# Optimization experiments

Measured on AMD Instinct MI355X. Metric: run time of the kernel, lower is better.

## Reference

```python
import jax, jax.numpy as jnp
import numpy as np

GRID = (128, 128, 128)
CENTER = np.array([0.0, 0.0, 0.0], dtype=np.float32)
SIZE = np.array([214.0, 214.0, 214.0], dtype=np.float32)
N_LORS = 65536
_CRYSTAL = SIZE[2] / GRID[2]
KERNEL_WIDTH = float(np.sqrt(_CRYSTAL * _CRYSTAL / np.pi))  # TOR gaussian sigma


def _make_lors(key, n, s):
    # rows: x1, y1, z1, x2, y2, z2 ; main direction along the 3rd coordinate
    k1, k2 = jax.random.split(key)
    trans = jax.random.uniform(k1, (4, n), jnp.float32, -0.45 * s, 0.45 * s)
    jit = jax.random.uniform(k2, (2, n), jnp.float32, -0.02 * s, 0.02 * s)
    half = 0.5 * s
    return jnp.stack([trans[0], trans[1], -half + jit[0],
                      trans[2], trans[3], half + jit[1]]).astype(jnp.float32)


def _project_bp(lors, image, grid, center, size, sigma):
    """TOR (tube-of-response) projection + listmode backprojection.
    lors: [N,6]; image shape == grid; main ray axis = last grid axis.
    Returns (line_integrals [N], backprojection volume grid)."""
    n0, n1, n2 = grid
    center = jnp.asarray(center, jnp.float32)
    size = jnp.asarray(size, jnp.float32)
    vox = size / jnp.array(grid, jnp.float32)
    xmin = center[0] - 0.5 * size[0]
    ymin = center[1] - 0.5 * size[1]
    zmin = center[2] - 0.5 * size[2]
    p1, p2 = lors[:, 0:3], lors[:, 3:6]
    d = p2 - p1
    L = jnp.sqrt(jnp.sum(d * d, axis=1))                    # [N]
    dz = d[:, 2]
    dz = jnp.where(jnp.abs(dz) < 1e-6, 1e-6, dz)
    zc = zmin + (jnp.arange(n2, dtype=jnp.float32) + 0.5) * vox[2]  # [K]
    t = (zc[None, :] - p1[:, 2:3]) / dz[:, None]            # [N,K] ray param per slice
    xs = p1[:, 0:1] + t * d[:, 0:1]                         # [N,K]
    ys = p1[:, 1:2] + t * d[:, 1:2]
    fi = (xs - xmin) / vox[0] - 0.5
    fj = (ys - ymin) / vox[1] - 0.5
    i0 = jnp.round(fi).astype(jnp.int32)
    j0 = jnp.round(fj).astype(jnp.int32)
    off = jnp.arange(-1, 2, dtype=jnp.int32)                # 3x3 in-plane TOR window
    oi = jnp.repeat(off, 3)                                  # [9]
    oj = jnp.tile(off, 3)                                    # [9]
    ii = i0[..., None] + oi                                  # [N,K,9]
    jj = j0[..., None] + oj
    inb = ((ii >= 0) & (ii < n0) & (jj >= 0) & (jj < n1)
           & (t[..., None] >= 0.0) & (t[..., None] <= 1.0))
    iic = jnp.clip(ii, 0, n0 - 1)
    jjc = jnp.clip(jj, 0, n1 - 1)
    dxv = (xmin + (iic.astype(jnp.float32) + 0.5) * vox[0]) - xs[..., None]
    dyv = (ymin + (jjc.astype(jnp.float32) + 0.5) * vox[1]) - ys[..., None]
    w = jnp.exp(-(dxv * dxv + dyv * dyv) / (2.0 * sigma * sigma))
    w = jnp.where(inb, w, 0.0)                               # [N,K,9]
    dl = vox[2] * L / jnp.abs(dz)                            # path length per slice [N]
    kk = jnp.broadcast_to(jnp.arange(n2, dtype=jnp.int32)[None, :, None], ii.shape)
    vals = image[iic, jjc, kk]                               # gather [N,K,9]
    proj = jnp.sum(w * vals, axis=(1, 2)) * dl               # [N]
    # listmode MLEM backprojection of 1/projection along same TOR weights
    contrib = w * (dl / (proj + 1e-8))[:, None, None]        # [N,K,9]
    flat = (iic * n1 + jjc) * n2 + kk
    bp = jnp.zeros(n0 * n1 * n2, jnp.float32).at[flat.reshape(-1)].add(
        contrib.reshape(-1)).reshape(n0, n1, n2)
    return proj, bp


def setup_inputs() -> dict:
    key = jax.random.key(0)
    kimg, keff, kx, ky, kz = jax.random.split(key, 5)
    image = jax.random.uniform(kimg, GRID, jnp.float32, 0.5, 1.5)
    effmap = jax.random.uniform(keff, GRID, jnp.float32, 0.5, 1.5)
    s = float(SIZE[0])
    return {
        'image': image,
        'efficiency_map': effmap,
        'xlors': _make_lors(kx, N_LORS, s),
        'ylors': _make_lors(ky, N_LORS, s),
        'zlors': _make_lors(kz, N_LORS, s),
    }


def reference(image, efficiency_map, xlors, ylors, zlors):
    g0, g1, g2 = GRID
    sigma = KERNEL_WIDTH
    imgz = image
    imgx = jnp.transpose(imgz, (2, 0, 1))
    imgy = jnp.transpose(imgz, (1, 0, 2))
    # stored as [6, N] -> [N, 6]
    xl, yl, zl = xlors.T, ylors.T, zlors.T
    pz, bpz = _project_bp(zl, imgz, GRID, CENTER, SIZE, sigma)
    gridx = (g0, g2, g1)
    px, bpx = _project_bp(xl, imgx, gridx, CENTER[[0, 2, 1]], SIZE[[0, 2, 1]], sigma)
    bpxt = jnp.transpose(bpx, (1, 2, 0))
    gridy = (g1, g2, g0)
    py, bpy = _project_bp(yl, imgy, gridy, CENTER[[1, 2, 0]], SIZE[[1, 2, 0]], sigma)
    bpyt = jnp.transpose(bpy, (1, 0, 2))
    return imgz / (efficiency_map + 1e-8) * (bpxt + bpyt + bpz)
```

## Files before the change

kernel.cpp:

```cpp
#include <hip/hip_runtime.h>
#include <hip/hip_fp16.h>
#include <math.h>

#define NLOR  65536
#define NG    128
#define PLANE (NG * NG)
#define NSUB  2
#define KG    8
#define NKG   (NG / KG)

#define VOX    1.671875f
#define XMIN  (-107.0f)
#define C2     1.57079632679f
#define C2L    2.26618007f

#define FPSCALE    8388608.0f
#define INVFPSCALE (1.0f / 8388608.0f)

#define PLP    129

#define PRM_STRIDE 8

typedef _Float16 h2v __attribute__((ext_vector_type(2)));

#if defined(__has_builtin)
#if __has_builtin(__builtin_amdgcn_fdot2)
#define HAVE_FDOT2 1
#endif
#endif

__device__ __forceinline__ float fdot2w(unsigned w, h2v wt, float c)
{
#ifdef HAVE_FDOT2
    return __builtin_amdgcn_fdot2(__builtin_bit_cast(h2v, w), wt, c, false);
#else
    const __half2 h = *reinterpret_cast<const __half2*>(&w);
    const float2 f = __half22float2(h);
    return c + (float)wt.x * f.x + (float)wt.y * f.y;
#endif
}

template<int SP, int SQ, int SR, int CONTIG>
__device__ __forceinline__ void permute_half_body(
    const float* __restrict__ in, __half* __restrict__ out,
    int b, float (*tile)[33])
{
    const int c0 = blockIdx.x * 32;
    const int r0 = blockIdx.y * 32;
    const int tx = threadIdx.x, ty = threadIdx.y;

#pragma unroll
    for (int m = 0; m < 4; ++m) {
        const int C = c0 + tx;
        const int R = r0 + ty + 8 * m;
        const int P = (CONTIG == 0) ? C : b;
        const int Q = (CONTIG == 0) ? b : C;
        tile[ty + 8 * m][tx] = in[P * SP + Q * SQ + R * SR];
    }
    __syncthreads();
#pragma unroll
    for (int m = 0; m < 4; ++m) {
        const int R = r0 + tx;
        const int C = c0 + ty + 8 * m;
        const int P = (CONTIG == 0) ? C : b;
        const int Q = (CONTIG == 0) ? b : C;
        const int o = P * PLANE + Q * NG + R;
        out[o] = __float2half(tile[tx][ty + 8 * m]);
    }
}

__global__ __launch_bounds__(256)
void perm_img2(const float* __restrict__ image,
               __half* __restrict__ imgPz, __half* __restrict__ imgPx,
               const float* __restrict__ zl, const float* __restrict__ yl,
               const float* __restrict__ xl,
               float* __restrict__ prmz, float* __restrict__ prmy,
               float* __restrict__ prmx)
{
    __shared__ float tile[32][33];
    const int b = blockIdx.z;
    if (b < 128) {
        permute_half_body<1, 16384, 128, 0>(image, imgPz, b, tile);
        return;
    }
    if (b < 256) {
        permute_half_body<128, 1, 16384, 1>(image, imgPx, b - 128, tile);
        return;
    }
    const int linear = (b - 256) * 16 + blockIdx.y * 4 + blockIdx.x;
    const int gid = linear * 256 + threadIdx.y * 32 + threadIdx.x;
    const int f   = gid >> 16;
    const int lor = gid & (NLOR - 1);
    const float* lors = (f == 0) ? zl : (f == 1) ? yl : xl;
    float* prm        = (f == 0) ? prmz : (f == 1) ? prmy : prmx;

    const float p1x = lors[0 * NLOR + lor];
    const float p1y = lors[1 * NLOR + lor];
    const float p1z = lors[2 * NLOR + lor];
    const float dx  = lors[3 * NLOR + lor] - p1x;
    const float dy  = lors[4 * NLOR + lor] - p1y;
    float dz = lors[5 * NLOR + lor] - p1z;
    dz = (fabsf(dz) < 1e-6f) ? 1e-6f : dz;
    const float rdz = 1.0f / dz;

    const float t0 = (XMIN + 0.5f * VOX - p1z) * rdz;
    const float dt = VOX * rdz;
    float u0 = (fmaf(t0, dx, p1x) - XMIN) * (1.0f / VOX) - 0.5f;
    float v0 = (fmaf(t0, dy, p1y) - XMIN) * (1.0f / VOX) - 0.5f;
    float du = dx * rdz;
    float dv = dy * rdz;
    if (f == 1) {
        float tmp = u0; u0 = v0; v0 = tmp;
        tmp = du; du = dv; dv = tmp;
    }
    float4* p4 = (float4*)(prm + (size_t)lor * PRM_STRIDE);
    p4[0] = make_float4(u0, du, v0, dv);
    p4[1] = make_float4(t0, dt, 0.0f, 0.0f);
}

template<int NS>
__device__ __forceinline__ void proj_body(
    const float* const* prmv, const unsigned int* __restrict__ imgP,
    float* const* p8v, unsigned int* plE, unsigned int* plO)
{
    const int g     = blockIdx.x;
    const int chunk = blockIdx.y;
    const int tid   = threadIdx.x;
    const int lor0  = chunk * 2048 + tid;
    const float k0  = (float)(g * KG);

    float tA[2 * NS], uA[2 * NS], vA[2 * NS], dtA[2 * NS], duA[2 * NS], dvA[2 * NS], sA[2 * NS];
#pragma unroll
    for (int s = 0; s < 2 * NS; ++s) {
        const float* prm = prmv[s >> 1];
        const int lor = lor0 + (s & 1) * 1024;
        const float4* p4 = (const float4*)(prm + (size_t)lor * PRM_STRIDE);
        const float4 a = p4[0];
        const float4 b = p4[1];
        tA[s] = fmaf(k0, b.y, b.x);  dtA[s] = b.y;
        uA[s] = fmaf(k0, a.y, a.x);  duA[s] = a.y;
        vA[s] = fmaf(k0, a.w, a.z);  dvA[s] = a.w;
        sA[s] = 0.0f;
    }

    for (int st = 0; st < KG; ++st) {
        const int k = g * KG + st;
        const unsigned* srcw = imgP + k * (NG * 64);
        const uint4* src = (const uint4*)srcw;
        uint4* dstE = (uint4*)plE;
        uint4* dstO = (uint4*)plO;
        for (int i = tid; i < (NG * 64) / 4; i += 1024) {
            const uint4 a = src[i];
            const unsigned nxt = srcw[4 * i + 4];
            uint4 o;
            o.x = (a.x >> 16) | (a.y << 16);
            o.y = (a.y >> 16) | (a.z << 16);
            o.z = (a.z >> 16) | (a.w << 16);
            o.w = (a.w >> 16) | (nxt << 16);
            dstE[i] = a;
            dstO[i] = o;
        }
        __syncthreads();

        const float fst = (float)st;
#pragma unroll
        for (int s = 0; s < 2 * NS; ++s) {
            const float t = fmaf(fst, dtA[s], tA[s]);
            const float u = fmaf(fst, duA[s], uA[s]);
            const float v = fmaf(fst, dvA[s], vA[s]);
            const float fi = rintf(u);
            const float fj = rintf(v);
            const int i0 = (int)fi;
            const int j0 = (int)fj;
            const float mi = fi - u;
            const float mj = fj - v;
            const float ci = -C2L * mi,  cj = -C2L * mj;
            const float a0i = ci * mi,   a0j = cj * mj;
            const float gi = ci + ci,    gj = cj + cj;
            const float ki = a0i - C2L,  kj = a0j - C2L;
            const float exm = __builtin_amdgcn_exp2f(ki - gi);
            const float ex0 = __builtin_amdgcn_exp2f(a0i);
            const float exq = __builtin_amdgcn_exp2f(ki + gi);
            const float eym = __builtin_amdgcn_exp2f(kj - gj);
            const float ey0 = __builtin_amdgcn_exp2f(a0j);
            const float eyq = __builtin_amdgcn_exp2f(kj + gj);

            h2v wLo; wLo.x = (_Float16)eym; wLo.y = (_Float16)ey0;
            h2v wHi; wHi.x = (_Float16)eyq; wHi.y = (_Float16)0.0f;

            const int w  = min(max((j0 - 1) >> 1, 0), 62);
            const int ib = min(max(i0 - 1, 0), 125);
            const unsigned* pp = (j0 & 1) ? plE : plO;

            const float exv[3] = {exm, ex0, exq};
            float acc = 0.0f;
#pragma unroll
            for (int a = 0; a < 3; ++a) {
                const int rowb = (ib + a) << 6;
                const unsigned Aw = pp[rowb + w];
                const unsigned Bw = pp[rowb + w + 1];
                float rd = fdot2w(Bw, wHi, 0.0f);
                rd = fdot2w(Aw, wLo, rd);
                acc = fmaf(exv[a], rd, acc);
            }
            const bool tin = (t >= 0.0f) && (t <= 1.0f);
            sA[s] += tin ? acc : 0.0f;
        }
        __syncthreads();
    }
#pragma unroll
    for (int s = 0; s < NS; ++s) {
        p8v[s][g * NLOR + lor0]        = sA[2 * s];
        p8v[s][g * NLOR + lor0 + 1024] = sA[2 * s + 1];
    }
}

__global__ __launch_bounds__(1024, 8)
void proj_all(const float* __restrict__ prmz, const float* __restrict__ prmy,
              const float* __restrict__ prmx,
              const unsigned int* __restrict__ imgPz, const unsigned int* __restrict__ imgPx,
              float* __restrict__ p8z, float* __restrict__ p8y,
              float* __restrict__ p8x)
{
    __shared__ unsigned int plE[NG * 64];
    __shared__ unsigned int plO[NG * 64];
    if (blockIdx.z == 0) {
        const float* prmv[2] = {prmz, prmy};
        float* p8v[2] = {p8z, p8y};
        proj_body<2>(prmv, imgPz, p8v, plE, plO);
    } else {
        const float* prmv[1] = {prmx};
        float* p8v[1] = {p8x};
        proj_body<1>(prmv, imgPx, p8v, plE, plO);
    }
}

__global__ __launch_bounds__(256)
void reduce_cf3(const float* __restrict__ zl, const float* __restrict__ yl,
                const float* __restrict__ xl,
                const float* __restrict__ p8z, const float* __restrict__ p8y,
                const float* __restrict__ p8x,
                float* __restrict__ prmz, float* __restrict__ prmy,
                float* __restrict__ prmx)
{
    const int which = blockIdx.y;
    const float* lors  = (which == 0) ? zl  : (which == 1) ? yl  : xl;
    const float* part8 = (which == 0) ? p8z : (which == 1) ? p8y : p8x;
    float*       prm   = (which == 0) ? prmz : (which == 1) ? prmy : prmx;

    const int lor = blockIdx.x * 256 + threadIdx.x;
    float s = 0.0f;
#pragma unroll
    for (int g = 0; g < NKG; ++g) s += part8[g * NLOR + lor];

    const float p1x = lors[0 * NLOR + lor];
    const float p1y = lors[1 * NLOR + lor];
    const float p1z = lors[2 * NLOR + lor];
    const float dx  = lors[3 * NLOR + lor] - p1x;
    const float dy  = lors[4 * NLOR + lor] - p1y;
    const float dz0 = lors[5 * NLOR + lor] - p1z;
    const float L = sqrtf(dx * dx + dy * dy + dz0 * dz0);
    const float adz = fmaxf(fabsf(dz0), 1e-6f);
    const float dl = VOX * L / adz;
    prm[(size_t)lor * PRM_STRIDE + 6] = (dl / (s * dl + 1e-8f)) * FPSCALE;
}

__device__ __forceinline__ void bp_deposit(const float* __restrict__ prm,
    int lor, float fk, unsigned int* __restrict__ pl)
{
    const float4* p4 = (const float4*)(prm + (size_t)lor * PRM_STRIDE);
    const float4 a = p4[0];
    const float4 b = p4[1];
    const float t = fmaf(fk, b.y, b.x);
    const float u = fmaf(fk, a.y, a.x);
    const float v = fmaf(fk, a.w, a.z);
    const float fi = rintf(u);
    const float fj = rintf(v);
    const float cfs = ((t >= 0.0f) && (t <= 1.0f)) ? b.z : 0.0f;

    const float mi = fi - u;
    const float mj = fj - v;
    const float ci = -C2L * mi,  cj = -C2L * mj;
    const float a0i = ci * mi,   a0j = cj * mj;
    const float gi = ci + ci,    gj = cj + cj;
    const float ki = a0i - C2L,  kj = a0j - C2L;

    const float ex0 = __builtin_amdgcn_exp2f(a0i) * cfs;
    const float exm = __builtin_amdgcn_exp2f(ki - gi) * cfs;
    const float exq = __builtin_amdgcn_exp2f(ki + gi) * cfs;
    const float ey0 = __builtin_amdgcn_exp2f(a0j);
    const float eym = __builtin_amdgcn_exp2f(kj - gj);
    const float eyq = __builtin_amdgcn_exp2f(kj + gj);

    const float fib = __builtin_amdgcn_fmed3f(fi, 1.0f, 126.0f);
    const float fjb = __builtin_amdgcn_fmed3f(fj, 1.0f, 126.0f);
    const int idx = (int)fmaf(fib, (float)PLP, fjb) - (PLP + 1);
    unsigned int* base = pl + idx;

    const float exv[3] = {exm, ex0, exq};
#pragma unroll
    for (int aa = 0; aa < 3; ++aa) {
        unsigned int* row = base + aa * PLP;
        atomicAdd(row + 0, (unsigned int)(exv[aa] * eym));
        atomicAdd(row + 1, (unsigned int)(exv[aa] * ey0));
        atomicAdd(row + 2, (unsigned int)(exv[aa] * eyq));
    }
}

__global__ __launch_bounds__(1024)
void bp_all(const float* __restrict__ prmz, const float* __restrict__ prmy,
            const float* __restrict__ prmx,
            float* __restrict__ bpA, float* __restrict__ bpB)
{
    __shared__ unsigned int pl[NG * PLP];
    const int k   = blockIdx.x >> 1;
    const int sub = blockIdx.x & 1;
    const int tid = threadIdx.x;

    for (int i = tid; i < NG * PLP; i += 1024) pl[i] = 0u;
    __syncthreads();

    const float fk = (float)k;
    const int lo = sub * (NLOR / NSUB);
    constexpr int NIT = (NLOR / NSUB) / 1024;
    float* bpsub;
    if (blockIdx.y == 0) {
#pragma unroll 2
        for (int it = 0; it < NIT; ++it) {
            const int lor = lo + tid + it * 1024;
            bp_deposit(prmz, lor, fk, pl);
            bp_deposit(prmy, lor, fk, pl);
        }
        bpsub = bpA;
    } else {
#pragma unroll 4
        for (int it = 0; it < NIT; ++it)
            bp_deposit(prmx, lo + tid + it * 1024, fk, pl);
        bpsub = bpB;
    }
    __syncthreads();

    float* dst = bpsub + ((size_t)(sub * NG + k)) * PLANE;
    for (int idx = tid; idx < PLANE; idx += 1024)
        dst[idx] = (float)pl[(idx & 127) * PLP + (idx >> 7)] * INVFPSCALE;
}

__global__ __launch_bounds__(256)
void finalize_out(const float* __restrict__ bpA, const float* __restrict__ bpB,
                  const float* __restrict__ img, const float* __restrict__ eff,
                  float* __restrict__ out)
{
    __shared__ float tA[32][33];
    const int b  = blockIdx.z;
    const int x0 = blockIdx.x * 32;
    const int z0 = blockIdx.y * 32;
    const int tx = threadIdx.x, ty = threadIdx.y;
    const int VOL = NG * PLANE;

#pragma unroll
    for (int m = 0; m < 4; ++m) {
        const int z = z0 + ty + 8 * m;
        const int a = z * PLANE + b * NG + (x0 + tx);
        tA[ty + 8 * m][tx] = bpA[a] + bpA[a + VOL];
    }
    __syncthreads();
#pragma unroll
    for (int m = 0; m < 4; ++m) {
        const int x  = x0 + ty + 8 * m;
        const int o  = x * PLANE + b * NG + (z0 + tx);
        const int bb = b * PLANE + x * NG + (z0 + tx);
        const float v = tA[tx][ty + 8 * m] + bpB[bb] + bpB[bb + VOL];
        out[o] = img[o] / (eff[o] + 1e-8f) * v;
    }
}

extern "C" void kernel_launch(void* const* d_in, const int* in_sizes, int n_in,
                              void* d_out, int out_size, void* d_ws, size_t ws_size,
                              hipStream_t stream) {
    const float* image = (const float*)d_in[0];
    const float* eff   = (const float*)d_in[1];
    const float* xl    = (const float*)d_in[2];
    const float* yl    = (const float*)d_in[3];
    const float* zl    = (const float*)d_in[4];
    float* out = (float*)d_out;

    char* ws = (char*)d_ws;
    __half* imgPz = (__half*)(ws);
    __half* imgPx = (__half*)(ws + (size_t)( 4 << 20));
    float* bpA    = (float*)(ws + (size_t)( 8 << 20));
    float* bpB    = (float*)(ws + (size_t)(24 << 20));
    float* p8z    = (float*)(ws + (size_t)(40 << 20));
    float* p8y    = (float*)(ws + (size_t)(44 << 20));
    float* p8x    = (float*)(ws + (size_t)(48 << 20));
    float* prmz   = (float*)(ws + (size_t)(52 << 20));
    float* prmy   = (float*)(ws + (size_t)(54 << 20));
    float* prmx   = (float*)(ws + (size_t)(56 << 20));

    const dim3 tb(32, 8);

    perm_img2<<<dim3(4, 4, 304), tb, 0, stream>>>(image, imgPz, imgPx,
        zl, yl, xl, prmz, prmy, prmx);
    proj_all<<<dim3(16, 32, 2), 1024, 0, stream>>>(prmz, prmy, prmx,
        (const unsigned int*)imgPz, (const unsigned int*)imgPx, p8z, p8y, p8x);
    reduce_cf3<<<dim3(256, 3), 256, 0, stream>>>(zl, yl, xl, p8z, p8y, p8x, prmz, prmy, prmx);
    bp_all<<<dim3(128 * NSUB, 2), 1024, 0, stream>>>(prmz, prmy, prmx, bpA, bpB);
    finalize_out<<<dim3(4, 4, 128), tb, 0, stream>>>(bpA, bpB, image, eff, out);
}
```

Before: 206.9 us.

## Drop odd-shifted plane copy and register-prefetch next slice during compute

Replaces the even/odd pair of shared-memory plane copies with a single plane. Odd/even column alignment is now handled by permuting the half-precision weights in registers. The next slice is prefetched from global memory into registers while the current slice is computed, so its load latency overlaps the dot-product work. This halves LDS usage and store traffic per slice, which could allow more resident blocks, at the cost of a few extra selects per LOR and one extra barrier per slice.

```diff
diff --git a/kernel.cpp b/kernel.cpp
--- a/kernel.cpp
+++ b/kernel.cpp
@@ -121,7 +121,7 @@
 template<int NS>
 __device__ __forceinline__ void proj_body(
     const float* const* prmv, const unsigned int* __restrict__ imgP,
-    float* const* p8v, unsigned int* plE, unsigned int* plO)
+    float* const* p8v, unsigned int* pl)
 {
     const int g     = blockIdx.x;
     const int chunk = blockIdx.y;
@@ -143,24 +143,24 @@
         sA[s] = 0.0f;
     }
 
+    uint4 pf0, pf1;
+    {
+        const uint4* src = (const uint4*)(imgP + (g * KG) * (NG * 64));
+        pf0 = src[tid];
+        pf1 = src[tid + 1024];
+    }
+
     for (int st = 0; st < KG; ++st) {
-        const int k = g * KG + st;
-        const unsigned* srcw = imgP + k * (NG * 64);
-        const uint4* src = (const uint4*)srcw;
-        uint4* dstE = (uint4*)plE;
-        uint4* dstO = (uint4*)plO;
-        for (int i = tid; i < (NG * 64) / 4; i += 1024) {
-            const uint4 a = src[i];
-            const unsigned nxt = srcw[4 * i + 4];
-            uint4 o;
-            o.x = (a.x >> 16) | (a.y << 16);
-            o.y = (a.y >> 16) | (a.z << 16);
-            o.z = (a.z >> 16) | (a.w << 16);
-            o.w = (a.w >> 16) | (nxt << 16);
-            dstE[i] = a;
-            dstO[i] = o;
+        __syncthreads();
+        uint4* dst = (uint4*)pl;
+        dst[tid]        = pf0;
+        dst[tid + 1024] = pf1;
+        __syncthreads();
+        if (st + 1 < KG) {
+            const uint4* src = (const uint4*)(imgP + (g * KG + st + 1) * (NG * 64));
+            pf0 = src[tid];
+            pf1 = src[tid + 1024];
         }
-        __syncthreads();
 
         const float fst = (float)st;
 #pragma unroll
@@ -185,20 +185,23 @@
             const float ey0 = __builtin_amdgcn_exp2f(a0j);
             const float eyq = __builtin_amdgcn_exp2f(kj + gj);
 
-            h2v wLo; wLo.x = (_Float16)eym; wLo.y = (_Float16)ey0;
-            h2v wHi; wHi.x = (_Float16)eyq; wHi.y = (_Float16)0.0f;
+            const _Float16 hm = (_Float16)eym, h0 = (_Float16)ey0,
+                           hq = (_Float16)eyq, hz = (_Float16)0.0f;
+            const bool odd = (j0 & 1) != 0;
+            h2v wLo, wHi;
+            wLo.x = odd ? hm : hz;  wLo.y = odd ? h0 : hm;
+            wHi.x = odd ? hq : h0;  wHi.y = odd ? hz : hq;
 
             const int w  = min(max((j0 - 1) >> 1, 0), 62);
             const int ib = min(max(i0 - 1, 0), 125);
-            const unsigned* pp = (j0 & 1) ? plE : plO;
 
             const float exv[3] = {exm, ex0, exq};
             float acc = 0.0f;
 #pragma unroll
             for (int a = 0; a < 3; ++a) {
                 const int rowb = (ib + a) << 6;
-                const unsigned Aw = pp[rowb + w];
-                const unsigned Bw = pp[rowb + w + 1];
+                const unsigned Aw = pl[rowb + w];
+                const unsigned Bw = pl[rowb + w + 1];
                 float rd = fdot2w(Bw, wHi, 0.0f);
                 rd = fdot2w(Aw, wLo, rd);
                 acc = fmaf(exv[a], rd, acc);
@@ -206,7 +209,6 @@
             const bool tin = (t >= 0.0f) && (t <= 1.0f);
             sA[s] += tin ? acc : 0.0f;
         }
-        __syncthreads();
     }
 #pragma unroll
     for (int s = 0; s < NS; ++s) {
@@ -222,16 +224,15 @@
               float* __restrict__ p8z, float* __restrict__ p8y,
               float* __restrict__ p8x)
 {
-    __shared__ unsigned int plE[NG * 64];
-    __shared__ unsigned int plO[NG * 64];
+    __shared__ unsigned int pl[NG * 64];
     if (blockIdx.z == 0) {
         const float* prmv[2] = {prmz, prmy};
         float* p8v[2] = {p8z, p8y};
-        proj_body<2>(prmv, imgPz, p8v, plE, plO);
+        proj_body<2>(prmv, imgPz, p8v, pl);
     } else {
         const float* prmv[1] = {prmx};
         float* p8v[1] = {p8x};
-        proj_body<1>(prmv, imgPx, p8v, plE, plO);
+        proj_body<1>(prmv, imgPx, p8v, pl);
     }
 }
 
```

New measurement: 195.3 us. 5.6% less time.
